# Performance work log

Measured on AMD Instinct MI355X. Metric: run time of the kernel, lower is better.

## Reference

```python
import jax, jax.numpy as jnp
import numpy as np

NS, N_ATOMS = 16, 2000
NB, NA, NV, NT, NI = 2000, 4000, 400000, 6000, 1000
CHARGE = 18.222615


def setup_inputs() -> dict:
    key = jax.random.key(0)
    ks = jax.random.split(key, 24)
    u = lambda k, s: jax.random.uniform(k, s, dtype=jnp.float32)
    n = lambda k, s: jax.random.normal(k, s, dtype=jnp.float32)
    return {
        'length_bond': 1.0 + 0.5 * u(ks[0], (NS, NB)),
        'theta_angle': 1.5 + 0.5 * u(ks[1], (NS, NA)),
        'length_vdw': 3.0 + 5.0 * u(ks[2], (NS, NV)),
        'sin_cos_torsion': n(ks[3], (NS, NT, 8)),
        'cos2_imptors': u(ks[4], (NS, NI)),
        'vdw14': 0.5 + 0.5 * u(ks[5], (NV,)),
        'charge14': 0.5 + 0.5 * u(ks[6], (NV,)),
        'paras_bond': 0.5 + u(ks[7], (NB, 2)),
        'paras_angle': 0.5 + u(ks[8], (NA, 2)),
        'paras_vdw': 0.5 + u(ks[9], (N_ATOMS, 2)),
        'paras_charge': 0.3 * n(ks[10], (N_ATOMS,)),
        'paras_torsion': 0.5 * n(ks[11], (NT, 4)),
        'paras_imptors': 0.5 + u(ks[12], (NI, 1)),
        'dlength_bond': n(ks[13], (NS, NB, 6)),
        'dtheta_angle': n(ks[14], (NS, NA, 9)),
        'dlength_vdw': n(ks[15], (NS, NV, 6)),
        'dtheta_torsion': n(ks[16], (NS, NT, 12)),
        'dcos2_imptors': n(ks[17], (NS, NI, 12)),
        'nonbonded': jax.random.randint(ks[18], (2, NV), 0, N_ATOMS),
        'bond_index': jax.random.randint(ks[19], (NB, 2), 0, N_ATOMS),
        'angle_index': jax.random.randint(ks[20], (NA, 3), 0, N_ATOMS),
        'nonbonded_index': jax.random.randint(ks[21], (NV, 2), 0, N_ATOMS),
        'torsion_index': jax.random.randint(ks[22], (NT, 4), 0, N_ATOMS),
        'imptors_index': jax.random.randint(ks[23], (NI, 4), 0, N_ATOMS),
    }


def reference(length_bond, theta_angle, length_vdw, sin_cos_torsion, cos2_imptors,
              vdw14, charge14, paras_bond, paras_angle, paras_vdw, paras_charge,
              paras_torsion, paras_imptors, dlength_bond, dtheta_angle, dlength_vdw,
              dtheta_torsion, dcos2_imptors, nonbonded, bond_index, angle_index,
              nonbonded_index, torsion_index, imptors_index):
    ns = length_bond.shape[0]
    n_atoms = paras_vdw.shape[0]
    # --- bond (harmonic; bond_morse=False) ---
    K = paras_bond[:, 0] * 100.0
    r0 = paras_bond[:, 1]
    d = length_bond - r0[None]                      # (ns, NB)
    E_bond = K[None] * d * d
    F_bond = (dlength_bond * (2.0 * K)[None, :, None] * d[:, :, None]).reshape(ns, -1, 3)
    # --- angle ---
    Ka = paras_angle[:, 0] * 10.0
    th0 = paras_angle[:, 1] * (np.pi / 10.0)
    da = theta_angle - th0[None]
    E_angle = Ka[None] * da * da
    F_angle = (dtheta_angle * (2.0 * Ka)[None, :, None] * da[:, :, None]).reshape(ns, -1, 3)
    # --- Urey-Bradley disabled (bool_ub=False) ---
    E_ub = jnp.zeros((ns, 1), dtype=length_bond.dtype)
    # --- van der Waals (LJ-like) ---
    i, j = nonbonded[0], nonbonded[1]
    sigma = paras_vdw[i, 0] + paras_vdw[j, 0]       # (NV,)
    eps = (paras_vdw[i, 1] / 10.0) * (paras_vdw[j, 1] / 10.0) * vdw14
    t = (sigma[None] ** 6) / (length_vdw ** 6)      # (ns, NV)
    E_vdw = eps[None] * (t * t - 2.0 * t)
    F_vdw = (dlength_vdw * (12.0 * eps)[None, :, None]
             * (t * (1.0 - t) / length_vdw)[:, :, None]).reshape(ns, -1, 3)
    # --- Coulomb ---
    c1 = (CHARGE / 10.0) * paras_charge[i]
    c2 = (CHARGE / 10.0) * paras_charge[j]
    cc = (c1 * c2 * charge14)[None]                 # (1, NV)
    E_charge = cc / length_vdw
    F_charge = (-dlength_vdw * (cc / (length_vdw ** 2))[:, :, None]).reshape(ns, -1, 3)
    # --- torsion (cos at channels 1,3,5,7; sin at 0,2,4,6) ---
    cosn = sin_cos_torsion[:, :, 1::2]              # (ns, NT, 4)
    sinn = sin_cos_torsion[:, :, 0::2]
    E_torsion = jnp.einsum('stn,tn->st', cosn, paras_torsion)
    coeff = paras_torsion * jnp.arange(1, 5, dtype=paras_torsion.dtype)[None]
    F_torsion = (-dtheta_torsion * jnp.einsum('stn,tn->st', sinn, coeff)[:, :, None]).reshape(ns, -1, 3)
    # --- improper torsion ---
    ki = paras_imptors[:, 0]
    E_imptors = ki[None] * (1.0 - cos2_imptors)
    F_imptors = (-dcos2_imptors * ki[None, :, None]).reshape(ns, -1, 3)
    # --- scatter-add all force contributions into per-atom Force ---
    Force = jnp.zeros((ns, n_atoms, 3), dtype=length_bond.dtype)
    Force = Force.at[:, bond_index.reshape(-1)].add(F_bond)
    Force = Force.at[:, angle_index.reshape(-1)].add(F_angle)
    Force = Force.at[:, nonbonded_index.reshape(-1)].add(F_vdw)
    Force = Force.at[:, nonbonded_index.reshape(-1)].add(F_charge)
    Force = Force.at[:, torsion_index.reshape(-1)].add(F_torsion)
    Force = Force.at[:, imptors_index.reshape(-1)].add(F_imptors)
    # Pack Energy dict entries + Force into one (ns, total) array
    return jnp.concatenate([E_bond, E_angle, E_ub, E_vdw, E_charge,
                            E_torsion, E_imptors, Force.reshape(ns, -1)], axis=1)
```

## Files before the change

### kernel.cpp

```cpp
#include <hip/hip_runtime.h>
#include <hip/hip_fp16.h>

#define NS 16
#define N_ATOMS 2000
#define NB 2000
#define NA 4000
#define NV 400000
#define NT 6000
#define NI 1000

#define OUT_S 819001
#define OFF_EB 0
#define OFF_EA 2000
#define OFF_EUB 6000
#define OFF_EV 6001
#define OFF_EC 406001
#define OFF_ET 806001
#define OFF_EI 812001
#define OFF_F 813001

#define CHARGE_TENTH 1.8222615f

#define NBF 44000
#define BF_BOND 0
#define BF_ANGLE 4000
#define BF_TORS 16000
#define BF_IMP 40000
#define NENTV (NV * 2)
#define NBOND_TOT (NB + NA + NT + NI)
#define NITEMS (NV + NB + NA + NT + NI)
#define NCB 64
#define IPB ((NITEMS + NCB - 1) / NCB)
#define VBLKS ((NV + 255) / 256)
#define BBH ((NBOND_TOT * 2 + 255) / 256)

typedef float f2v __attribute__((ext_vector_type(2)));

__device__ __forceinline__ unsigned pkrtz(float a, float b) {
    typedef __fp16 hv2 __attribute__((ext_vector_type(2)));
    hv2 h = __builtin_amdgcn_cvt_pkrtz(a, b);
    return __builtin_bit_cast(unsigned, h);
}

__global__ __launch_bounds__(256, 4) void inithist_kernel(
    const float* __restrict__ v14, const float* __restrict__ q14,
    const float* __restrict__ pv, const float* __restrict__ pc,
    const int* __restrict__ nb,
    const int* __restrict__ nbi, const int* __restrict__ bidx,
    const int* __restrict__ aidx, const int* __restrict__ tidx,
    const int* __restrict__ iidx,
    float4* __restrict__ ws, int* __restrict__ countsV, int* __restrict__ countsB,
    float* __restrict__ out)
{
    __shared__ int hV[N_ATOMS];
    __shared__ int hB[N_ATOMS];
    int tid = threadIdx.x, b = blockIdx.x;

    if (b >= NCB) {
        int idx = (b - NCB) * 256 + tid;
        if (idx < NS) out[(size_t)idx * OUT_S + OFF_EUB] = 0.0f;
        if (idx < NV) {
            int v = idx;
            int i = nb[v];
            int j = nb[NV + v];
            float2 pvi = ((const float2*)pv)[i];
            float2 pvj = ((const float2*)pv)[j];
            float sigma = pvi.x + pvj.x;
            float sig2 = sigma * sigma;
            float4 w;
            w.x = sig2 * sig2 * sig2;
            w.y = pvi.y * pvj.y * 0.01f * v14[v];
            w.z = (CHARGE_TENTH * CHARGE_TENTH) * pc[i] * pc[j] * q14[v];
            w.w = 0.0f;
            ws[v] = w;
        }
        return;
    }

    for (int k = tid; k < N_ATOMS; k += 256) { hV[k] = 0; hB[k] = 0; }
    __syncthreads();
    int t0 = b * IPB, t1 = t0 + IPB; if (t1 > NITEMS) t1 = NITEMS;
    for (int t = t0 + tid; t < t1; t += 256) {
        if (t < NV) {
            atomicAdd(&hV[nbi[2 * t]], 1);
            atomicAdd(&hV[nbi[2 * t + 1]], 1);
        } else if (t < NV + NB) {
            int x = t - NV;
            atomicAdd(&hB[bidx[2 * x]], 1);
            atomicAdd(&hB[bidx[2 * x + 1]], 1);
        } else if (t < NV + NB + NA) {
            int x = t - (NV + NB);
            atomicAdd(&hB[aidx[3 * x]], 1);
            atomicAdd(&hB[aidx[3 * x + 1]], 1);
            atomicAdd(&hB[aidx[3 * x + 2]], 1);
        } else if (t < NV + NB + NA + NT) {
            int x = t - (NV + NB + NA);
            #pragma unroll
            for (int p = 0; p < 4; ++p) atomicAdd(&hB[tidx[4 * x + p]], 1);
        } else {
            int x = t - (NV + NB + NA + NT);
            #pragma unroll
            for (int p = 0; p < 4; ++p) atomicAdd(&hB[iidx[4 * x + p]], 1);
        }
    }
    __syncthreads();
    for (int k = tid; k < N_ATOMS; k += 256) {
        countsV[(size_t)b * N_ATOMS + k] = hV[k];
        countsB[(size_t)b * N_ATOMS + k] = hB[k];
    }
}

__global__ __launch_bounds__(256) void colscan2_kernel(
    int* __restrict__ countsV, int* __restrict__ countsB,
    int* __restrict__ totalV, int* __restrict__ totalB)
{
    int a = blockIdx.x * 256 + threadIdx.x;
    if (a < N_ATOMS) {
        int pre = 0;
        for (int b = 0; b < NCB; ++b) {
            int c = countsV[(size_t)b * N_ATOMS + a];
            countsV[(size_t)b * N_ATOMS + a] = pre;
            pre += c;
        }
        totalV[a] = pre;
    } else if (a < 2 * N_ATOMS) {
        int aa = a - N_ATOMS;
        int pre = 0;
        for (int b = 0; b < NCB; ++b) {
            int c = countsB[(size_t)b * N_ATOMS + aa];
            countsB[(size_t)b * N_ATOMS + aa] = pre;
            pre += c;
        }
        totalB[aa] = pre;
    }
}

__device__ __forceinline__ void wave_scan(const int* __restrict__ total,
                                          int* __restrict__ startx, int lane)
{
    const int CH = (N_ATOMS + 63) / 64;
    int a0 = lane * CH, a1 = a0 + CH; if (a1 > N_ATOMS) a1 = N_ATOMS;
    int tot = 0;
    for (int a = a0; a < a1; ++a) tot += total[a];
    int incl = tot;
    #pragma unroll
    for (int off = 1; off < 64; off <<= 1) {
        int n = __shfl_up(incl, off);
        if (lane >= off) incl += n;
    }
    int run = incl - tot;
    for (int a = a0; a < a1; ++a) { startx[a] = run; run += total[a]; }
    if (lane == 63) startx[N_ATOMS] = run;
}

__global__ __launch_bounds__(64) void scan2_kernel(
    const int* __restrict__ totalV, const int* __restrict__ totalB,
    int* __restrict__ startxV, int* __restrict__ startxB)
{
    int lane = threadIdx.x;
    wave_scan(totalV, startxV, lane);
    wave_scan(totalB, startxB, lane);
}

__global__ __launch_bounds__(256, 4) void place2_kernel(
    const int* __restrict__ nbi, const int* __restrict__ bidx,
    const int* __restrict__ aidx, const int* __restrict__ tidx,
    const int* __restrict__ iidx,
    const int* __restrict__ countsV, const int* __restrict__ countsB,
    const int* __restrict__ startxV, const int* __restrict__ startxB,
    int* __restrict__ posv, int* __restrict__ posb)
{
    __shared__ int curV[N_ATOMS];
    __shared__ int curB[N_ATOMS];
    int tid = threadIdx.x, b = blockIdx.x;
    for (int k = tid; k < N_ATOMS; k += 256) {
        curV[k] = startxV[k] + countsV[(size_t)b * N_ATOMS + k];
        curB[k] = startxB[k] + countsB[(size_t)b * N_ATOMS + k];
    }
    __syncthreads();
    int t0 = b * IPB, t1 = t0 + IPB; if (t1 > NITEMS) t1 = NITEMS;
    for (int t = t0 + tid; t < t1; t += 256) {
        if (t < NV) {
            posv[2 * t]     = atomicAdd(&curV[nbi[2 * t]], 1);
            posv[2 * t + 1] = atomicAdd(&curV[nbi[2 * t + 1]], 1);
        } else if (t < NV + NB) {
            int x = t - NV;
            #pragma unroll
            for (int sl = 0; sl < 2; ++sl)
                posb[BF_BOND + x * 2 + sl] = atomicAdd(&curB[bidx[2 * x + sl]], 1);
        } else if (t < NV + NB + NA) {
            int x = t - (NV + NB);
            #pragma unroll
            for (int sl = 0; sl < 3; ++sl)
                posb[BF_ANGLE + x * 3 + sl] = atomicAdd(&curB[aidx[3 * x + sl]], 1);
        } else if (t < NV + NB + NA + NT) {
            int x = t - (NV + NB + NA);
            #pragma unroll
            for (int sl = 0; sl < 4; ++sl)
                posb[BF_TORS + x * 4 + sl] = atomicAdd(&curB[tidx[4 * x + sl]], 1);
        } else {
            int x = t - (NV + NB + NA + NT);
            #pragma unroll
            for (int sl = 0; sl < 4; ++sl)
                posb[BF_IMP + x * 4 + sl] = atomicAdd(&curB[iidx[4 * x + sl]], 1);
        }
    }
}

__global__ __launch_bounds__(256, 4) void work_kernel(
    const float* __restrict__ lv, const float* __restrict__ dlv,
    const float4* __restrict__ ws, const int* __restrict__ posv,
    const float* __restrict__ lb, const float* __restrict__ th,
    const float* __restrict__ sc, const float* __restrict__ c2i,
    const float* __restrict__ pb, const float* __restrict__ pa,
    const float* __restrict__ pt, const float* __restrict__ pim,
    const float* __restrict__ dlb, const float* __restrict__ dth,
    const float* __restrict__ dtt, const float* __restrict__ dc2,
    const int* __restrict__ posb,
    unsigned* __restrict__ cV, unsigned* __restrict__ cB,
    float* __restrict__ out)
{
    int x = blockIdx.x;
    int tid = threadIdx.x;

    if (x >= BBH) {
        int v = (x - BBH) * 256 + tid;
        if (v >= NV) return;
        float4 w = ws[v];
        int2 pp = *(const int2*)(posv + 2 * v);
        unsigned cp[24];
        float hold[3][6];
        #pragma unroll
        for (int s = 0; s < 16; ++s) {
            float r = lv[(size_t)s * NV + v];
            const float2* d2 = (const float2*)(dlv + ((size_t)s * NV + v) * 6);
            float2 dA = d2[0], dB = d2[1], dC = d2[2];
            float rinv = __builtin_amdgcn_rcpf(r);
            float r2inv = rinv * rinv;
            float r6inv = r2inv * r2inv * r2inv;
            float t = w.x * r6inv;
            out[(size_t)s * OUT_S + OFF_EV + v] = w.y * (t * t - 2.0f * t);
            out[(size_t)s * OUT_S + OFF_EC + v] = w.z * rinv;
            float fsv = 12.0f * w.y * t * (1.0f - t) * rinv - w.z * r2inv;
            float cc[6];
            cc[0] = dA.x * fsv; cc[1] = dA.y * fsv; cc[2] = dB.x * fsv;
            cc[3] = dB.y * fsv; cc[4] = dC.x * fsv; cc[5] = dC.y * fsv;
            int m = s & 3;
            if (m < 3) {
                #pragma unroll
                for (int k = 0; k < 6; ++k) hold[m][k] = cc[k];
            } else {
                int q = s >> 2;
                #pragma unroll
                for (int k = 0; k < 6; ++k) {
                    int t0 = __builtin_amdgcn_cvt_pk_fp8_f32(hold[0][k], hold[1][k], 0, false);
                    t0 = __builtin_amdgcn_cvt_pk_fp8_f32(hold[2][k], cc[k], t0, true);
                    cp[(k / 3) * 12 + (k % 3) * 4 + q] = (unsigned)t0;
                }
            }
        }
        uint4* dst0 = (uint4*)(cV + (size_t)pp.x * 12);
        #pragma unroll
        for (int k = 0; k < 3; ++k)
            dst0[k] = make_uint4(cp[4 * k], cp[4 * k + 1], cp[4 * k + 2], cp[4 * k + 3]);
        uint4* dst1 = (uint4*)(cV + (size_t)pp.y * 12);
        #pragma unroll
        for (int k = 0; k < 3; ++k)
            dst1[k] = make_uint4(cp[12 + 4 * k], cp[12 + 4 * k + 1], cp[12 + 4 * k + 2], cp[12 + 4 * k + 3]);
        return;
    }

    int idx = x * 256 + tid;
    int h = idx & 1;
    int t = idx >> 1;
    if (t >= NBOND_TOT) return;
    int sbase = h * 8;

    if (t < NB) {
        int b = t;
        float2 p = ((const float2*)pb)[b];
        float K = p.x * 100.0f;
        unsigned cp[24]; float hold[6];
        #pragma unroll
        for (int j = 0; j < 8; ++j) {
            int s = sbase + j;
            float d = lb[s * NB + b] - p.y;
            out[(size_t)s * OUT_S + OFF_EB + b] = K * d * d;
            float g = 2.0f * K * d;
            const float2* dd = (const float2*)(dlb + ((size_t)s * NB + b) * 6);
            float2 dA = dd[0], dB = dd[1], dC = dd[2];
            float v0 = dA.x * g, v1 = dA.y * g, v2 = dB.x * g;
            float v3 = dB.y * g, v4 = dC.x * g, v5 = dC.y * g;
            if ((j & 1) == 0) { hold[0]=v0; hold[1]=v1; hold[2]=v2; hold[3]=v3; hold[4]=v4; hold[5]=v5; }
            else {
                int q = j >> 1;
                cp[0*12 + 0*4 + q] = pkrtz(hold[0], v0);
                cp[0*12 + 1*4 + q] = pkrtz(hold[1], v1);
                cp[0*12 + 2*4 + q] = pkrtz(hold[2], v2);
                cp[1*12 + 0*4 + q] = pkrtz(hold[3], v3);
                cp[1*12 + 1*4 + q] = pkrtz(hold[4], v4);
                cp[1*12 + 2*4 + q] = pkrtz(hold[5], v5);
            }
        }
        #pragma unroll
        for (int sl = 0; sl < 2; ++sl) {
            uint4* dst = (uint4*)(cB + (size_t)posb[BF_BOND + b * 2 + sl] * 24 + h * 12);
            #pragma unroll
            for (int k = 0; k < 3; ++k)
                dst[k] = make_uint4(cp[sl*12+4*k], cp[sl*12+4*k+1], cp[sl*12+4*k+2], cp[sl*12+4*k+3]);
        }
    } else if (t < NB + NA) {
        int a = t - NB;
        float2 p = ((const float2*)pa)[a];
        float Ka = p.x * 10.0f;
        float th0 = p.y * 0.31415926535f;
        unsigned cp[36]; float hold[9];
        #pragma unroll
        for (int j = 0; j < 8; ++j) {
            int s = sbase + j;
            float da = th[s * NA + a] - th0;
            out[(size_t)s * OUT_S + OFF_EA + a] = Ka * da * da;
            float g = 2.0f * Ka * da;
            const float* dd = dth + ((size_t)s * NA + a) * 9;
            float v[9];
            #pragma unroll
            for (int k = 0; k < 9; ++k) v[k] = dd[k] * g;
            if ((j & 1) == 0) {
                #pragma unroll
                for (int k = 0; k < 9; ++k) hold[k] = v[k];
            } else {
                int q = j >> 1;
                #pragma unroll
                for (int k = 0; k < 9; ++k)
                    cp[(k / 3) * 12 + (k % 3) * 4 + q] = pkrtz(hold[k], v[k]);
            }
        }
        #pragma unroll
        for (int sl = 0; sl < 3; ++sl) {
            uint4* dst = (uint4*)(cB + (size_t)posb[BF_ANGLE + a * 3 + sl] * 24 + h * 12);
            #pragma unroll
            for (int k = 0; k < 3; ++k)
                dst[k] = make_uint4(cp[sl*12+4*k], cp[sl*12+4*k+1], cp[sl*12+4*k+2], cp[sl*12+4*k+3]);
        }
    } else if (t < NB + NA + NT) {
        int tt = t - (NB + NA);
        float4 p4 = ((const float4*)pt)[tt];
        unsigned cp[48]; float hold[12];
        #pragma unroll
        for (int j = 0; j < 8; ++j) {
            int s = sbase + j;
            const float4* s8 = (const float4*)(sc + ((size_t)s * NT + tt) * 8);
            float4 sA = s8[0], sB = s8[1];
            out[(size_t)s * OUT_S + OFF_ET + tt] =
                sA.y * p4.x + sA.w * p4.y + sB.y * p4.z + sB.w * p4.w;
            float g = -(sA.x * p4.x + sA.z * p4.y * 2.0f + sB.x * p4.z * 3.0f + sB.z * p4.w * 4.0f);
            const float4* dd = (const float4*)(dtt + ((size_t)s * NT + tt) * 12);
            float4 dA = dd[0], dB = dd[1], dC = dd[2];
            float v[12] = {dA.x*g, dA.y*g, dA.z*g, dA.w*g, dB.x*g, dB.y*g,
                           dB.z*g, dB.w*g, dC.x*g, dC.y*g, dC.z*g, dC.w*g};
            if ((j & 1) == 0) {
                #pragma unroll
                for (int k = 0; k < 12; ++k) hold[k] = v[k];
            } else {
                int q = j >> 1;
                #pragma unroll
                for (int k = 0; k < 12; ++k)
                    cp[(k / 3) * 12 + (k % 3) * 4 + q] = pkrtz(hold[k], v[k]);
            }
        }
        #pragma unroll
        for (int sl = 0; sl < 4; ++sl) {
            uint4* dst = (uint4*)(cB + (size_t)posb[BF_TORS + tt * 4 + sl] * 24 + h * 12);
            #pragma unroll
            for (int k = 0; k < 3; ++k)
                dst[k] = make_uint4(cp[sl*12+4*k], cp[sl*12+4*k+1], cp[sl*12+4*k+2], cp[sl*12+4*k+3]);
        }
    } else {
        int ii = t - (NB + NA + NT);
        float ki = pim[ii];
        float g = -ki;
        unsigned cp[48]; float hold[12];
        #pragma unroll
        for (int j = 0; j < 8; ++j) {
            int s = sbase + j;
            out[(size_t)s * OUT_S + OFF_EI + ii] = ki * (1.0f - c2i[s * NI + ii]);
            const float4* dd = (const float4*)(dc2 + ((size_t)s * NI + ii) * 12);
            float4 dA = dd[0], dB = dd[1], dC = dd[2];
            float v[12] = {dA.x*g, dA.y*g, dA.z*g, dA.w*g, dB.x*g, dB.y*g,
                           dB.z*g, dB.w*g, dC.x*g, dC.y*g, dC.z*g, dC.w*g};
            if ((j & 1) == 0) {
                #pragma unroll
                for (int k = 0; k < 12; ++k) hold[k] = v[k];
            } else {
                int q = j >> 1;
                #pragma unroll
                for (int k = 0; k < 12; ++k)
                    cp[(k / 3) * 12 + (k % 3) * 4 + q] = pkrtz(hold[k], v[k]);
            }
        }
        #pragma unroll
        for (int sl = 0; sl < 4; ++sl) {
            uint4* dst = (uint4*)(cB + (size_t)posb[BF_IMP + ii * 4 + sl] * 24 + h * 12);
            #pragma unroll
            for (int k = 0; k < 3; ++k)
                dst[k] = make_uint4(cp[sl*12+4*k], cp[sl*12+4*k+1], cp[sl*12+4*k+2], cp[sl*12+4*k+3]);
        }
    }
}

__global__ __launch_bounds__(256, 2) void gather2_kernel(
    const unsigned* __restrict__ cV, const unsigned* __restrict__ cB,
    const int* __restrict__ startxV, const int* __restrict__ startxB,
    float* __restrict__ out)
{
    __shared__ float red[4][48];
    int wv = threadIdx.x >> 6, lane = threadIdx.x & 63;
    int a0 = blockIdx.x * 4;
    int a = a0 + wv;

    float acc[48];
    #pragma unroll
    for (int k = 0; k < 48; ++k) acc[k] = 0.0f;

    {
        int base = startxV[a], endp = startxV[a + 1];
        for (int i = base + lane; i < endp; i += 64) {
            const uint4* e = (const uint4*)(cV + (size_t)i * 12);
            uint4 q0 = e[0], q1 = e[1], q2 = e[2];
            unsigned wd[12] = {q0.x, q0.y, q0.z, q0.w,
                               q1.x, q1.y, q1.z, q1.w,
                               q2.x, q2.y, q2.z, q2.w};
            #pragma unroll
            for (int wi = 0; wi < 12; ++wi) {
                int comp = wi >> 2, q = wi & 3;
                f2v lo = __builtin_amdgcn_cvt_pk_f32_fp8(wd[wi], false);
                f2v hi = __builtin_amdgcn_cvt_pk_f32_fp8(wd[wi], true);
                acc[comp * 16 + 4 * q + 0] += lo.x;
                acc[comp * 16 + 4 * q + 1] += lo.y;
                acc[comp * 16 + 4 * q + 2] += hi.x;
                acc[comp * 16 + 4 * q + 3] += hi.y;
            }
        }
    }
    {
        int base = startxB[a], endp = startxB[a + 1];
        for (int i = base + lane; i < endp; i += 64) {
            const uint4* e = (const uint4*)(cB + (size_t)i * 24);
            uint4 q0 = e[0], q1 = e[1], q2 = e[2], q3 = e[3], q4 = e[4], q5 = e[5];
            unsigned wd[24] = {q0.x, q0.y, q0.z, q0.w, q1.x, q1.y, q1.z, q1.w,
                               q2.x, q2.y, q2.z, q2.w, q3.x, q3.y, q3.z, q3.w,
                               q4.x, q4.y, q4.z, q4.w, q5.x, q5.y, q5.z, q5.w};
            #pragma unroll
            for (int wi = 0; wi < 24; ++wi) {
                int h = wi / 12, rem = wi - h * 12;
                int comp = rem >> 2, qq = rem & 3;
                int s0 = h * 8 + 2 * qq;
                __half2 hh = __builtin_bit_cast(__half2, wd[wi]);
                acc[comp * 16 + s0]     += __low2float(hh);
                acc[comp * 16 + s0 + 1] += __high2float(hh);
            }
        }
    }

    #pragma unroll
    for (int off = 32; off > 0; off >>= 1) {
        #pragma unroll
        for (int k = 0; k < 48; ++k)
            acc[k] += __shfl_down(acc[k], off);
    }
    if (lane == 0) {
        #pragma unroll
        for (int k = 0; k < 48; ++k) red[wv][k] = acc[k];
    }
    __syncthreads();
    int th = threadIdx.x;
    if (th < 192) {
        int s = th / 12, idx = th % 12;
        int ai = idx / 3, comp = idx % 3;
        out[(size_t)s * OUT_S + OFF_F + 3 * (a0 + ai) + comp] = red[ai][comp * 16 + s];
    }
}

extern "C" void kernel_launch(void* const* d_in, const int* in_sizes, int n_in,
                              void* d_out, int out_size, void* d_ws, size_t ws_size,
                              hipStream_t stream) {
    const float* lb  = (const float*)d_in[0];
    const float* th  = (const float*)d_in[1];
    const float* lv  = (const float*)d_in[2];
    const float* sc  = (const float*)d_in[3];
    const float* c2i = (const float*)d_in[4];
    const float* v14 = (const float*)d_in[5];
    const float* q14 = (const float*)d_in[6];
    const float* pb  = (const float*)d_in[7];
    const float* pa  = (const float*)d_in[8];
    const float* pv  = (const float*)d_in[9];
    const float* pc  = (const float*)d_in[10];
    const float* pt  = (const float*)d_in[11];
    const float* pim = (const float*)d_in[12];
    const float* dlb = (const float*)d_in[13];
    const float* dth = (const float*)d_in[14];
    const float* dlv = (const float*)d_in[15];
    const float* dtt = (const float*)d_in[16];
    const float* dc2 = (const float*)d_in[17];
    const int* nb    = (const int*)d_in[18];
    const int* bidx  = (const int*)d_in[19];
    const int* aidx  = (const int*)d_in[20];
    const int* nbi   = (const int*)d_in[21];
    const int* tidx  = (const int*)d_in[22];
    const int* iidx  = (const int*)d_in[23];
    float* out = (float*)d_out;

    unsigned* cV      = (unsigned*)d_ws;
    unsigned* cB      = cV + (size_t)NENTV * 12;
    float4*   wsp     = (float4*)(cB + (size_t)NBF * 24);
    int*      posv    = (int*)(wsp + NV);
    int*      posb    = posv + 2 * NV;
    int*      countsV = posb + NBF;
    int*      countsB = countsV + (size_t)NCB * N_ATOMS;
    int*      totalV  = countsB + (size_t)NCB * N_ATOMS;
    int*      totalB  = totalV + N_ATOMS;
    int*      startxV = totalB + N_ATOMS;
    int*      startxB = startxV + (N_ATOMS + 1);

    inithist_kernel<<<NCB + VBLKS, 256, 0, stream>>>(
        v14, q14, pv, pc, nb, nbi, bidx, aidx, tidx, iidx,
        wsp, countsV, countsB, out);
    colscan2_kernel<<<(2 * N_ATOMS + 255) / 256, 256, 0, stream>>>(countsV, countsB, totalV, totalB);
    scan2_kernel<<<1, 64, 0, stream>>>(totalV, totalB, startxV, startxB);
    place2_kernel<<<NCB, 256, 0, stream>>>(nbi, bidx, aidx, tidx, iidx,
                                           countsV, countsB, startxV, startxB, posv, posb);
    work_kernel<<<BBH + VBLKS, 256, 0, stream>>>(
        lv, dlv, wsp, posv, lb, th, sc, c2i, pb, pa, pt, pim,
        dlb, dth, dtt, dc2, posb, cV, cB, out);
    gather2_kernel<<<N_ATOMS / 4, 256, 0, stream>>>(cV, cB, startxV, startxB, out);
}
```

Before: 140.7 us.

## Split nonbonded work into two kernels, stage derivative loads via LDS, pad entries

Splits the nonbonded force work in half. The first half runs in a dedicated kernel that preloads all 16 samples before computing. The second half stays in the bonded kernel and loads dlength_vdw as coalesced float4 per wavefront, staged through shared memory. Per-pair compressed force entries are padded from 48 to 64 bytes for aligned writes and gathers, and the histogram block count is halved. This trades extra write bandwidth from padding, an extra launch and higher register pressure for better load coalescing and memory-level parallelism.

New measurement: 192.0 us. +36.5%, slower.

```diff
diff --git a/kernel.cpp b/kernel.cpp
--- a/kernel.cpp
+++ b/kernel.cpp
@@ -29,9 +29,10 @@
 #define NENTV (NV * 2)
 #define NBOND_TOT (NB + NA + NT + NI)
 #define NITEMS (NV + NB + NA + NT + NI)
-#define NCB 64
+#define NCB 32
 #define IPB ((NITEMS + NCB - 1) / NCB)
-#define VBLKS ((NV + 255) / 256)
+#define NVH (NV / 2)
+#define VBLKH ((NVH + 255) / 256)
 #define BBH ((NBOND_TOT * 2 + 255) / 256)
 
 typedef float f2v __attribute__((ext_vector_type(2)));
@@ -207,7 +208,71 @@
     }
 }
 
-__global__ __launch_bounds__(256, 4) void work_kernel(
+__device__ __forceinline__ void phaseA_body(
+    int v, float r[16], float2 dA[16], float2 dB[16], float2 dC[16],
+    float4 w, int2 pp, unsigned* __restrict__ cV, float* __restrict__ out)
+{
+    unsigned cp[24];
+    float hold[3][6];
+    #pragma unroll
+    for (int s = 0; s < 16; ++s) {
+        float rinv = __builtin_amdgcn_rcpf(r[s]);
+        float r2inv = rinv * rinv;
+        float r6inv = r2inv * r2inv * r2inv;
+        float t = w.x * r6inv;
+        out[(size_t)s * OUT_S + OFF_EV + v] = w.y * (t * t - 2.0f * t);
+        out[(size_t)s * OUT_S + OFF_EC + v] = w.z * rinv;
+        float fsv = 12.0f * w.y * t * (1.0f - t) * rinv - w.z * r2inv;
+        float cc[6];
+        cc[0] = dA[s].x * fsv; cc[1] = dA[s].y * fsv; cc[2] = dB[s].x * fsv;
+        cc[3] = dB[s].y * fsv; cc[4] = dC[s].x * fsv; cc[5] = dC[s].y * fsv;
+        int m = s & 3;
+        if (m < 3) {
+            #pragma unroll
+            for (int k = 0; k < 6; ++k) hold[m][k] = cc[k];
+        } else {
+            int q = s >> 2;
+            #pragma unroll
+            for (int k = 0; k < 6; ++k) {
+                int t0 = __builtin_amdgcn_cvt_pk_fp8_f32(hold[0][k], hold[1][k], 0, false);
+                t0 = __builtin_amdgcn_cvt_pk_fp8_f32(hold[2][k], cc[k], t0, true);
+                cp[(k / 3) * 12 + (k % 3) * 4 + q] = (unsigned)t0;
+            }
+        }
+    }
+    uint4 zero = make_uint4(0u, 0u, 0u, 0u);
+    uint4* dst0 = (uint4*)(cV + (size_t)pp.x * 16);
+    #pragma unroll
+    for (int k = 0; k < 3; ++k)
+        dst0[k] = make_uint4(cp[4 * k], cp[4 * k + 1], cp[4 * k + 2], cp[4 * k + 3]);
+    dst0[3] = zero;
+    uint4* dst1 = (uint4*)(cV + (size_t)pp.y * 16);
+    #pragma unroll
+    for (int k = 0; k < 3; ++k)
+        dst1[k] = make_uint4(cp[12 + 4 * k], cp[12 + 4 * k + 1], cp[12 + 4 * k + 2], cp[12 + 4 * k + 3]);
+    dst1[3] = zero;
+}
+
+__global__ __launch_bounds__(256, 4) void workA_kernel(
+    const float* __restrict__ lv, const float* __restrict__ dlv,
+    const float4* __restrict__ ws, const int* __restrict__ posv,
+    unsigned* __restrict__ cV, float* __restrict__ out)
+{
+    int v = blockIdx.x * 256 + threadIdx.x;
+    if (v >= NVH) return;
+    float4 w = ws[v];
+    int2 pp = *(const int2*)(posv + 2 * v);
+    float r[16]; float2 dA[16], dB[16], dC[16];
+    #pragma unroll
+    for (int s = 0; s < 16; ++s) {
+        const float2* d2 = (const float2*)(dlv + ((size_t)s * NV + v) * 6);
+        dA[s] = d2[0]; dB[s] = d2[1]; dC[s] = d2[2];
+        r[s] = lv[(size_t)s * NV + v];
+    }
+    phaseA_body(v, r, dA, dB, dC, w, pp, cV, out);
+}
+
+__global__ __launch_bounds__(256, 4) void workB_kernel(
     const float* __restrict__ lv, const float* __restrict__ dlv,
     const float4* __restrict__ ws, const int* __restrict__ posv,
     const float* __restrict__ lb, const float* __restrict__ th,
@@ -220,53 +285,36 @@
     unsigned* __restrict__ cV, unsigned* __restrict__ cB,
     float* __restrict__ out)
 {
+    __shared__ float4 stage[4][96];
     int x = blockIdx.x;
     int tid = threadIdx.x;
 
     if (x >= BBH) {
-        int v = (x - BBH) * 256 + tid;
-        if (v >= NV) return;
+        int wv = tid >> 6, lane = tid & 63;
+        int vbase = NVH + (x - BBH) * 256 + wv * 64;
+        if (vbase >= NV) return;
+        int v = vbase + lane;
         float4 w = ws[v];
         int2 pp = *(const int2*)(posv + 2 * v);
-        unsigned cp[24];
-        float hold[3][6];
+        float4* st = stage[wv];
+        const float4* dfl4 = (const float4*)dlv;
+        float r[16]; float2 dA[16], dB[16], dC[16];
         #pragma unroll
         for (int s = 0; s < 16; ++s) {
-            float r = lv[(size_t)s * NV + v];
-            const float2* d2 = (const float2*)(dlv + ((size_t)s * NV + v) * 6);
-            float2 dA = d2[0], dB = d2[1], dC = d2[2];
-            float rinv = __builtin_amdgcn_rcpf(r);
-            float r2inv = rinv * rinv;
-            float r6inv = r2inv * r2inv * r2inv;
-            float t = w.x * r6inv;
-            out[(size_t)s * OUT_S + OFF_EV + v] = w.y * (t * t - 2.0f * t);
-            out[(size_t)s * OUT_S + OFF_EC + v] = w.z * rinv;
-            float fsv = 12.0f * w.y * t * (1.0f - t) * rinv - w.z * r2inv;
-            float cc[6];
-            cc[0] = dA.x * fsv; cc[1] = dA.y * fsv; cc[2] = dB.x * fsv;
-            cc[3] = dB.y * fsv; cc[4] = dC.x * fsv; cc[5] = dC.y * fsv;
-            int m = s & 3;
-            if (m < 3) {
-                #pragma unroll
-                for (int k = 0; k < 6; ++k) hold[m][k] = cc[k];
-            } else {
-                int q = s >> 2;
-                #pragma unroll
-                for (int k = 0; k < 6; ++k) {
-                    int t0 = __builtin_amdgcn_cvt_pk_fp8_f32(hold[0][k], hold[1][k], 0, false);
-                    t0 = __builtin_amdgcn_cvt_pk_fp8_f32(hold[2][k], cc[k], t0, true);
-                    cp[(k / 3) * 12 + (k % 3) * 4 + q] = (unsigned)t0;
-                }
-            }
-        }
-        uint4* dst0 = (uint4*)(cV + (size_t)pp.x * 12);
-        #pragma unroll
-        for (int k = 0; k < 3; ++k)
-            dst0[k] = make_uint4(cp[4 * k], cp[4 * k + 1], cp[4 * k + 2], cp[4 * k + 3]);
-        uint4* dst1 = (uint4*)(cV + (size_t)pp.y * 12);
-        #pragma unroll
-        for (int k = 0; k < 3; ++k)
-            dst1[k] = make_uint4(cp[12 + 4 * k], cp[12 + 4 * k + 1], cp[12 + 4 * k + 2], cp[12 + 4 * k + 3]);
+            size_t f4base = ((size_t)s * NV + vbase) / 2 * 3;
+            float4 t0 = dfl4[f4base + lane];
+            float4 t1;
+            if (lane < 32) t1 = dfl4[f4base + 64 + lane];
+            st[lane] = t0;
+            if (lane < 32) st[64 + lane] = t1;
+            asm volatile("s_waitcnt lgkmcnt(0)" ::: "memory");
+            const float2* stp = (const float2*)st;
+            dA[s] = stp[lane * 3];
+            dB[s] = stp[lane * 3 + 1];
+            dC[s] = stp[lane * 3 + 2];
+            r[s] = lv[(size_t)s * NV + v];
+        }
+        phaseA_body(v, r, dA, dB, dC, w, pp, cV, out);
         return;
     }
 
@@ -425,7 +473,7 @@
     {
         int base = startxV[a], endp = startxV[a + 1];
         for (int i = base + lane; i < endp; i += 64) {
-            const uint4* e = (const uint4*)(cV + (size_t)i * 12);
+            const uint4* e = (const uint4*)(cV + (size_t)i * 16);
             uint4 q0 = e[0], q1 = e[1], q2 = e[2];
             unsigned wd[12] = {q0.x, q0.y, q0.z, q0.w,
                                q1.x, q1.y, q1.z, q1.w,
@@ -511,7 +559,7 @@
     float* out = (float*)d_out;
 
     unsigned* cV      = (unsigned*)d_ws;
-    unsigned* cB      = cV + (size_t)NENTV * 12;
+    unsigned* cB      = cV + (size_t)NENTV * 16;
     float4*   wsp     = (float4*)(cB + (size_t)NBF * 24);
     int*      posv    = (int*)(wsp + NV);
     int*      posb    = posv + 2 * NV;
@@ -522,14 +570,15 @@
     int*      startxV = totalB + N_ATOMS;
     int*      startxB = startxV + (N_ATOMS + 1);
 
-    inithist_kernel<<<NCB + VBLKS, 256, 0, stream>>>(
+    inithist_kernel<<<NCB + (NV + 255) / 256, 256, 0, stream>>>(
         v14, q14, pv, pc, nb, nbi, bidx, aidx, tidx, iidx,
         wsp, countsV, countsB, out);
     colscan2_kernel<<<(2 * N_ATOMS + 255) / 256, 256, 0, stream>>>(countsV, countsB, totalV, totalB);
     scan2_kernel<<<1, 64, 0, stream>>>(totalV, totalB, startxV, startxB);
     place2_kernel<<<NCB, 256, 0, stream>>>(nbi, bidx, aidx, tidx, iidx,
                                            countsV, countsB, startxV, startxB, posv, posb);
-    work_kernel<<<BBH + VBLKS, 256, 0, stream>>>(
+    workA_kernel<<<VBLKH, 256, 0, stream>>>(lv, dlv, wsp, posv, cV, out);
+    workB_kernel<<<BBH + VBLKH, 256, 0, stream>>>(
         lv, dlv, wsp, posv, lb, th, sc, c2i, pb, pa, pt, pim,
         dlb, dth, dtt, dc2, posb, cV, cB, out);
     gather2_kernel<<<N_ATOMS / 4, 256, 0, stream>>>(cV, cB, startxV, startxB, out);
```

## Move VdW force compute into histogram kernel and gather via index list

Applied to the files above, without the earlier changes.

The nonbonded energy and force computation now runs in the first kernel, alongside the histogram blocks, and writes fp8-packed per-entry forces in input order (padded to 64 bytes) instead of to sorted positions. The placement kernel now emits a per-atom list of entry indices, and the gather kernel reads its contributions indirectly through that list. This removes the float4 parameter workspace round trip, lets the heavy streaming work overlap with the histogram and scan phases, and shrinks the last compute kernel to bonded terms only. The cost is an extra indirection and scattered 64-byte reads in the gather, plus larger padded entries.

Measured after the change: 144.9 us. 1.03x slower.

```diff
diff --git a/kernel.cpp b/kernel.cpp
--- a/kernel.cpp
+++ b/kernel.cpp
@@ -42,14 +42,16 @@
     return __builtin_bit_cast(unsigned, h);
 }
 
-__global__ __launch_bounds__(256, 4) void inithist_kernel(
+__global__ __launch_bounds__(256, 4) void histA_kernel(
+    const float* __restrict__ lv, const float* __restrict__ dlv,
     const float* __restrict__ v14, const float* __restrict__ q14,
     const float* __restrict__ pv, const float* __restrict__ pc,
     const int* __restrict__ nb,
     const int* __restrict__ nbi, const int* __restrict__ bidx,
     const int* __restrict__ aidx, const int* __restrict__ tidx,
     const int* __restrict__ iidx,
-    float4* __restrict__ ws, int* __restrict__ countsV, int* __restrict__ countsB,
+    unsigned* __restrict__ cV,
+    int* __restrict__ countsV, int* __restrict__ countsB,
     float* __restrict__ out)
 {
     __shared__ int hV[N_ATOMS];
@@ -57,23 +59,62 @@
     int tid = threadIdx.x, b = blockIdx.x;
 
     if (b >= NCB) {
-        int idx = (b - NCB) * 256 + tid;
-        if (idx < NS) out[(size_t)idx * OUT_S + OFF_EUB] = 0.0f;
-        if (idx < NV) {
-            int v = idx;
-            int i = nb[v];
-            int j = nb[NV + v];
-            float2 pvi = ((const float2*)pv)[i];
-            float2 pvj = ((const float2*)pv)[j];
-            float sigma = pvi.x + pvj.x;
-            float sig2 = sigma * sigma;
-            float4 w;
-            w.x = sig2 * sig2 * sig2;
-            w.y = pvi.y * pvj.y * 0.01f * v14[v];
-            w.z = (CHARGE_TENTH * CHARGE_TENTH) * pc[i] * pc[j] * q14[v];
-            w.w = 0.0f;
-            ws[v] = w;
-        }
+        int v = (b - NCB) * 256 + tid;
+        if (v >= NV) return;
+        if (v < NS) out[(size_t)v * OUT_S + OFF_EUB] = 0.0f;
+
+        int i = nb[v];
+        int j = nb[NV + v];
+        float2 pvi = ((const float2*)pv)[i];
+        float2 pvj = ((const float2*)pv)[j];
+        float sigma = pvi.x + pvj.x;
+        float sig2 = sigma * sigma;
+        float sig6 = sig2 * sig2 * sig2;
+        float eps  = pvi.y * pvj.y * 0.01f * v14[v];
+        float ccq  = (CHARGE_TENTH * CHARGE_TENTH) * pc[i] * pc[j] * q14[v];
+
+        unsigned cp[24];
+        float hold[3][6];
+        #pragma unroll
+        for (int s = 0; s < 16; ++s) {
+            float r = lv[(size_t)s * NV + v];
+            const float2* d2 = (const float2*)(dlv + ((size_t)s * NV + v) * 6);
+            float2 dA = d2[0], dB = d2[1], dC = d2[2];
+            float rinv = __builtin_amdgcn_rcpf(r);
+            float r2inv = rinv * rinv;
+            float r6inv = r2inv * r2inv * r2inv;
+            float t = sig6 * r6inv;
+            out[(size_t)s * OUT_S + OFF_EV + v] = eps * (t * t - 2.0f * t);
+            out[(size_t)s * OUT_S + OFF_EC + v] = ccq * rinv;
+            float fsv = 12.0f * eps * t * (1.0f - t) * rinv - ccq * r2inv;
+            float cc[6];
+            cc[0] = dA.x * fsv; cc[1] = dA.y * fsv; cc[2] = dB.x * fsv;
+            cc[3] = dB.y * fsv; cc[4] = dC.x * fsv; cc[5] = dC.y * fsv;
+            int m = s & 3;
+            if (m < 3) {
+                #pragma unroll
+                for (int k = 0; k < 6; ++k) hold[m][k] = cc[k];
+            } else {
+                int q = s >> 2;
+                #pragma unroll
+                for (int k = 0; k < 6; ++k) {
+                    int t0i = __builtin_amdgcn_cvt_pk_fp8_f32(hold[0][k], hold[1][k], 0, false);
+                    t0i = __builtin_amdgcn_cvt_pk_fp8_f32(hold[2][k], cc[k], t0i, true);
+                    cp[(k / 3) * 12 + (k % 3) * 4 + q] = (unsigned)t0i;
+                }
+            }
+        }
+        uint4 zero = make_uint4(0u, 0u, 0u, 0u);
+        uint4* dst0 = (uint4*)(cV + (size_t)(2 * v) * 16);
+        dst0[0] = make_uint4(cp[0], cp[1], cp[2], cp[3]);
+        dst0[1] = make_uint4(cp[4], cp[5], cp[6], cp[7]);
+        dst0[2] = make_uint4(cp[8], cp[9], cp[10], cp[11]);
+        dst0[3] = zero;
+        uint4* dst1 = (uint4*)(cV + (size_t)(2 * v + 1) * 16);
+        dst1[0] = make_uint4(cp[12], cp[13], cp[14], cp[15]);
+        dst1[1] = make_uint4(cp[16], cp[17], cp[18], cp[19]);
+        dst1[2] = make_uint4(cp[20], cp[21], cp[22], cp[23]);
+        dst1[3] = zero;
         return;
     }
 
@@ -168,7 +209,7 @@
     const int* __restrict__ iidx,
     const int* __restrict__ countsV, const int* __restrict__ countsB,
     const int* __restrict__ startxV, const int* __restrict__ startxB,
-    int* __restrict__ posv, int* __restrict__ posb)
+    unsigned* __restrict__ entries, int* __restrict__ posb)
 {
     __shared__ int curV[N_ATOMS];
     __shared__ int curB[N_ATOMS];
@@ -181,8 +222,10 @@
     int t0 = b * IPB, t1 = t0 + IPB; if (t1 > NITEMS) t1 = NITEMS;
     for (int t = t0 + tid; t < t1; t += 256) {
         if (t < NV) {
-            posv[2 * t]     = atomicAdd(&curV[nbi[2 * t]], 1);
-            posv[2 * t + 1] = atomicAdd(&curV[nbi[2 * t + 1]], 1);
+            int p0 = atomicAdd(&curV[nbi[2 * t]], 1);
+            entries[p0] = (unsigned)(2 * t);
+            int p1 = atomicAdd(&curV[nbi[2 * t + 1]], 1);
+            entries[p1] = (unsigned)(2 * t + 1);
         } else if (t < NV + NB) {
             int x = t - NV;
             #pragma unroll
@@ -207,9 +250,7 @@
     }
 }
 
-__global__ __launch_bounds__(256, 4) void work_kernel(
-    const float* __restrict__ lv, const float* __restrict__ dlv,
-    const float4* __restrict__ ws, const int* __restrict__ posv,
+__global__ __launch_bounds__(256, 4) void bondedc_kernel(
     const float* __restrict__ lb, const float* __restrict__ th,
     const float* __restrict__ sc, const float* __restrict__ c2i,
     const float* __restrict__ pb, const float* __restrict__ pa,
@@ -217,60 +258,9 @@
     const float* __restrict__ dlb, const float* __restrict__ dth,
     const float* __restrict__ dtt, const float* __restrict__ dc2,
     const int* __restrict__ posb,
-    unsigned* __restrict__ cV, unsigned* __restrict__ cB,
-    float* __restrict__ out)
-{
-    int x = blockIdx.x;
-    int tid = threadIdx.x;
-
-    if (x >= BBH) {
-        int v = (x - BBH) * 256 + tid;
-        if (v >= NV) return;
-        float4 w = ws[v];
-        int2 pp = *(const int2*)(posv + 2 * v);
-        unsigned cp[24];
-        float hold[3][6];
-        #pragma unroll
-        for (int s = 0; s < 16; ++s) {
-            float r = lv[(size_t)s * NV + v];
-            const float2* d2 = (const float2*)(dlv + ((size_t)s * NV + v) * 6);
-            float2 dA = d2[0], dB = d2[1], dC = d2[2];
-            float rinv = __builtin_amdgcn_rcpf(r);
-            float r2inv = rinv * rinv;
-            float r6inv = r2inv * r2inv * r2inv;
-            float t = w.x * r6inv;
-            out[(size_t)s * OUT_S + OFF_EV + v] = w.y * (t * t - 2.0f * t);
-            out[(size_t)s * OUT_S + OFF_EC + v] = w.z * rinv;
-            float fsv = 12.0f * w.y * t * (1.0f - t) * rinv - w.z * r2inv;
-            float cc[6];
-            cc[0] = dA.x * fsv; cc[1] = dA.y * fsv; cc[2] = dB.x * fsv;
-            cc[3] = dB.y * fsv; cc[4] = dC.x * fsv; cc[5] = dC.y * fsv;
-            int m = s & 3;
-            if (m < 3) {
-                #pragma unroll
-                for (int k = 0; k < 6; ++k) hold[m][k] = cc[k];
-            } else {
-                int q = s >> 2;
-                #pragma unroll
-                for (int k = 0; k < 6; ++k) {
-                    int t0 = __builtin_amdgcn_cvt_pk_fp8_f32(hold[0][k], hold[1][k], 0, false);
-                    t0 = __builtin_amdgcn_cvt_pk_fp8_f32(hold[2][k], cc[k], t0, true);
-                    cp[(k / 3) * 12 + (k % 3) * 4 + q] = (unsigned)t0;
-                }
-            }
-        }
-        uint4* dst0 = (uint4*)(cV + (size_t)pp.x * 12);
-        #pragma unroll
-        for (int k = 0; k < 3; ++k)
-            dst0[k] = make_uint4(cp[4 * k], cp[4 * k + 1], cp[4 * k + 2], cp[4 * k + 3]);
-        uint4* dst1 = (uint4*)(cV + (size_t)pp.y * 12);
-        #pragma unroll
-        for (int k = 0; k < 3; ++k)
-            dst1[k] = make_uint4(cp[12 + 4 * k], cp[12 + 4 * k + 1], cp[12 + 4 * k + 2], cp[12 + 4 * k + 3]);
-        return;
-    }
-
-    int idx = x * 256 + tid;
+    unsigned* __restrict__ cB, float* __restrict__ out)
+{
+    int idx = blockIdx.x * 256 + threadIdx.x;
     int h = idx & 1;
     int t = idx >> 1;
     if (t >= NBOND_TOT) return;
@@ -410,6 +400,7 @@
 
 __global__ __launch_bounds__(256, 2) void gather2_kernel(
     const unsigned* __restrict__ cV, const unsigned* __restrict__ cB,
+    const unsigned* __restrict__ entries,
     const int* __restrict__ startxV, const int* __restrict__ startxB,
     float* __restrict__ out)
 {
@@ -425,8 +416,9 @@
     {
         int base = startxV[a], endp = startxV[a + 1];
         for (int i = base + lane; i < endp; i += 64) {
-            const uint4* e = (const uint4*)(cV + (size_t)i * 12);
-            uint4 q0 = e[0], q1 = e[1], q2 = e[2];
+            unsigned e = entries[i];
+            const uint4* ep = (const uint4*)(cV + (size_t)e * 16);
+            uint4 q0 = ep[0], q1 = ep[1], q2 = ep[2];
             unsigned wd[12] = {q0.x, q0.y, q0.z, q0.w,
                                q1.x, q1.y, q1.z, q1.w,
                                q2.x, q2.y, q2.z, q2.w};
@@ -511,10 +503,9 @@
     float* out = (float*)d_out;
 
     unsigned* cV      = (unsigned*)d_ws;
-    unsigned* cB      = cV + (size_t)NENTV * 12;
-    float4*   wsp     = (float4*)(cB + (size_t)NBF * 24);
-    int*      posv    = (int*)(wsp + NV);
-    int*      posb    = posv + 2 * NV;
+    unsigned* cB      = cV + (size_t)NENTV * 16;
+    unsigned* entries = cB + (size_t)NBF * 24;
+    int*      posb    = (int*)(entries + NENTV);
     int*      countsV = posb + NBF;
     int*      countsB = countsV + (size_t)NCB * N_ATOMS;
     int*      totalV  = countsB + (size_t)NCB * N_ATOMS;
@@ -522,15 +513,14 @@
     int*      startxV = totalB + N_ATOMS;
     int*      startxB = startxV + (N_ATOMS + 1);
 
-    inithist_kernel<<<NCB + VBLKS, 256, 0, stream>>>(
-        v14, q14, pv, pc, nb, nbi, bidx, aidx, tidx, iidx,
-        wsp, countsV, countsB, out);
+    histA_kernel<<<NCB + VBLKS, 256, 0, stream>>>(
+        lv, dlv, v14, q14, pv, pc, nb, nbi, bidx, aidx, tidx, iidx,
+        cV, countsV, countsB, out);
     colscan2_kernel<<<(2 * N_ATOMS + 255) / 256, 256, 0, stream>>>(countsV, countsB, totalV, totalB);
     scan2_kernel<<<1, 64, 0, stream>>>(totalV, totalB, startxV, startxB);
     place2_kernel<<<NCB, 256, 0, stream>>>(nbi, bidx, aidx, tidx, iidx,
-                                           countsV, countsB, startxV, startxB, posv, posb);
-    work_kernel<<<BBH + VBLKS, 256, 0, stream>>>(
-        lv, dlv, wsp, posv, lb, th, sc, c2i, pb, pa, pt, pim,
-        dlb, dth, dtt, dc2, posb, cV, cB, out);
-    gather2_kernel<<<N_ATOMS / 4, 256, 0, stream>>>(cV, cB, startxV, startxB, out);
-}
+                                           countsV, countsB, startxV, startxB, entries, posb);
+    bondedc_kernel<<<BBH, 256, 0, stream>>>(lb, th, sc, c2i, pb, pa, pt, pim,
+                                            dlb, dth, dtt, dc2, posb, cB, out);
+    gather2_kernel<<<N_ATOMS / 4, 256, 0, stream>>>(cV, cB, entries, startxV, startxB, out);
+}
```
